# Optimization experiments

Measured on AMD Instinct MI355X. Metric: run time of the kernel, lower is better.

Reference implementation:

```python
import jax, jax.numpy as jnp
import numpy as np

P = 512       # protein_dim
D = 512       # drug_dim
N = 2000      # neighbors per layer
E = 300000    # binding edges per layer
ND = 100000   # total drugs
BASELINE = 6.0
LN_EPS = 1e-5


def setup_inputs() -> dict:
    key = jax.random.key(0)
    ks = jax.random.split(key, 24)
    inp = {
        "target_features": jax.random.normal(ks[0], (P,), jnp.float32),
        "form_features": jax.random.normal(ks[1], (N, P), jnp.float32),
        "role_features": jax.random.normal(ks[2], (N, P), jnp.float32),
        "form_neighbors": jnp.arange(N, dtype=jnp.int64) if jax.config.jax_enable_x64 else jnp.arange(N, dtype=jnp.int32),
        "role_neighbors": jnp.arange(N, dtype=jnp.int32),
        "form_binds_ei": jax.random.randint(ks[3], (2, E), 0, N, jnp.int32),
        "form_binds_y": jax.random.uniform(ks[4], (E,), jnp.float32) * 8.0 + 2.0,
        "role_binds_ei": jax.random.randint(ks[5], (2, E), 0, N, jnp.int32),
        "role_binds_y": jax.random.uniform(ks[6], (E,), jnp.float32) * 8.0 + 2.0,
        "drug_features": jax.random.normal(ks[7], (ND, D), jnp.float32),
    }
    inp["form_neighbors"] = jnp.arange(N, dtype=jnp.int32)
    attn_in = P * 2 + 16
    s1 = 1.0 / np.sqrt(attn_in)
    s2 = 1.0 / np.sqrt(64)
    sd = 1.0 / np.sqrt(D)
    sp = 1.0 / np.sqrt(P)
    inp["layer_emb"] = jax.random.normal(ks[8], (2, 16), jnp.float32)
    inp["W1"] = jax.random.uniform(ks[9], (attn_in, 64), jnp.float32, -s1, s1)
    inp["b1"] = jax.random.uniform(ks[10], (64,), jnp.float32, -s1, s1)
    inp["W2"] = jax.random.uniform(ks[11], (64, 1), jnp.float32, -s2, s2)
    inp["b2"] = jax.random.uniform(ks[12], (1,), jnp.float32, -s2, s2)
    inp["Wi1"] = jax.random.uniform(ks[13], (D, P), jnp.float32, -sd, sd)
    inp["bi1"] = jax.random.uniform(ks[14], (P,), jnp.float32, -sd, sd)
    inp["prelu_alpha"] = jnp.array(0.25, jnp.float32)
    inp["Wi2"] = jax.random.uniform(ks[15], (P, P), jnp.float32, -sp, sp)
    inp["bi2"] = jax.random.uniform(ks[16], (P,), jnp.float32, -sp, sp)
    inp["ln_gamma"] = jnp.ones((P,), jnp.float32)
    inp["ln_beta"] = jnp.zeros((P,), jnp.float32)
    return inp


def _pref_vectors(neighbor_ids, ei, y, drug_features):
    # Vectorized form of the per-neighbor masked gather-sum:
    # for each edge, find its neighbor slot (neighbor_ids is sorted);
    # edges whose src id is not a neighbor get zero weight.
    n = neighbor_ids.shape[0]
    pos = jnp.clip(jnp.searchsorted(neighbor_ids, ei[0]), 0, n - 1)
    valid = neighbor_ids[pos] == ei[0]
    w = jnp.where(valid, y - BASELINE, 0.0)              # [E]
    contrib = drug_features[ei[1]] * w[:, None]          # [E, D] gather (memory-bound)
    return jax.ops.segment_sum(contrib, pos, num_segments=n)  # [N, D]


def _attention(z_target, z_neighbors, l_vec, W1, b1, W2, b2):
    n = z_neighbors.shape[0]
    inp = jnp.concatenate(
        [jnp.broadcast_to(z_target, (n, z_target.shape[0])),
         z_neighbors,
         jnp.broadcast_to(l_vec, (n, l_vec.shape[0]))], axis=-1)  # [N, 2P+16]
    h = inp @ W1 + b1
    h = jnp.where(h > 0, h, 0.2 * h)  # LeakyReLU(0.2)
    return h @ W2 + b2                # [N, 1]


def reference(target_features, form_features, role_features, form_neighbors,
              role_neighbors, form_binds_ei, form_binds_y, role_binds_ei,
              role_binds_y, drug_features, layer_emb, W1, b1, W2, b2,
              Wi1, bi1, prelu_alpha, Wi2, bi2, ln_gamma, ln_beta):
    form_msgs = _pref_vectors(form_neighbors, form_binds_ei, form_binds_y, drug_features)
    role_msgs = _pref_vectors(role_neighbors, role_binds_ei, role_binds_y, drug_features)

    form_attn = _attention(target_features, form_features, layer_emb[0], W1, b1, W2, b2)
    role_attn = _attention(target_features, role_features, layer_emb[1], W1, b1, W2, b2)

    all_msgs = jnp.concatenate([form_msgs, role_msgs], axis=0)   # [2N, D]
    all_attn = jnp.concatenate([form_attn, role_attn], axis=0)   # [2N, 1]
    attn_weights = jax.nn.softmax(all_attn, axis=0)
    v_prior = jnp.sum(attn_weights * all_msgs, axis=0)           # [D]

    h = v_prior @ Wi1 + bi1
    h = jnp.where(h > 0, h, prelu_alpha * h)  # PReLU
    v = h @ Wi2 + bi2                          # [P]

    x = target_features + v
    mu = jnp.mean(x)
    var = jnp.mean(jnp.square(x - mu))
    z_refined = (x - mu) / jnp.sqrt(var + LN_EPS) * ln_gamma + ln_beta
    return (z_refined, form_msgs, role_msgs)
```

## Files before the change

### kernel.cpp

```cpp
#include <hip/hip_runtime.h>
#include <math.h>

static constexpr int PD = 512;
static constexpr float BASEV = 6.0f;
static constexpr int CAP = 320;

__global__ __launch_bounds__(256) void front_kernel(
    const int* __restrict__ ei_f, const float* __restrict__ y_f,
    const int* __restrict__ ei_r, const float* __restrict__ y_r,
    const int* __restrict__ nb_f, const int* __restrict__ nb_r,
    const float* __restrict__ target, const float* __restrict__ formF,
    const float* __restrict__ roleF, const float* __restrict__ lemb,
    const float* __restrict__ W1, const float* __restrict__ b1,
    const float* __restrict__ W2, const float* __restrict__ b2,
    int N, int E, int eb,
    int* __restrict__ cnt, int2* __restrict__ bins,
    float* __restrict__ logits) {
    int b = blockIdx.x;
    if (b < eb) {
        int i = b * 256 + threadIdx.x;
        if (i >= 2 * E) return;
        bool role = i >= E;
        int e = role ? i - E : i;
        const int* ei0 = role ? ei_r : ei_f;
        const int* ei1 = (role ? ei_r : ei_f) + E;
        int v = ei0[e];
        const int* nb = role ? nb_r : nb_f;
        int lo = 0, hi = N;
        while (lo < hi) { int mid = (lo + hi) >> 1; if (nb[mid] < v) lo = mid + 1; else hi = mid; }
        int pos = lo < N ? lo : N - 1;
        if (nb[pos] != v) return;
        int s = role ? N + pos : pos;
        float w = (role ? y_r[e] : y_f[e]) - BASEV;
        int slot = atomicAdd(&cnt[s], 1);
        if (slot < CAP) bins[(size_t)s * CAP + slot] = make_int2(ei1[e], __float_as_int(w));
    } else {
        int wave = threadIdx.x >> 6, lane = threadIdx.x & 63;
        int r0 = ((b - eb) * 4 + wave) * 8;
        int nseg = 2 * N;
        if (r0 >= nseg) return;
        const float* W1t = W1 + lane;
        float c = b1[lane];
        const float4* t4 = (const float4*)target;
        for (int p = 0; p < PD; p += 4) {
            float4 tv = t4[p >> 2];
            c += tv.x * W1t[(size_t)(p + 0) * 64] + tv.y * W1t[(size_t)(p + 1) * 64]
               + tv.z * W1t[(size_t)(p + 2) * 64] + tv.w * W1t[(size_t)(p + 3) * 64];
        }
        float c0 = c, c1 = c;
        for (int q = 0; q < 16; q++) {
            float wq = W1t[(size_t)(2 * PD + q) * 64];
            c0 += lemb[q] * wq;
            c1 += lemb[16 + q] * wq;
        }
        int nrows = nseg - r0; if (nrows > 8) nrows = 8;
        const float* z[8];
        float h[8];
#pragma unroll
        for (int r = 0; r < 8; r++) {
            int rr = r0 + (r < nrows ? r : 0);
            bool rl = rr >= N;
            z[r] = rl ? roleF + (size_t)(rr - N) * PD : formF + (size_t)rr * PD;
            h[r] = rl ? c1 : c0;
        }
        const float* W1z = W1 + (size_t)PD * 64 + lane;
        for (int p = 0; p < PD; p += 4) {
            float w0 = W1z[(size_t)(p + 0) * 64], w1 = W1z[(size_t)(p + 1) * 64];
            float w2 = W1z[(size_t)(p + 2) * 64], w3 = W1z[(size_t)(p + 3) * 64];
#pragma unroll
            for (int r = 0; r < 8; r++) {
                float4 zv = *(const float4*)(z[r] + p);
                h[r] += zv.x * w0 + zv.y * w1 + zv.z * w2 + zv.w * w3;
            }
        }
        float w2l = W2[lane];
#pragma unroll
        for (int r = 0; r < 8; r++) {
            float hh = h[r];
            hh = hh > 0.f ? hh : 0.2f * hh;
            float vv = hh * w2l;
#pragma unroll
            for (int off = 32; off > 0; off >>= 1) vv += __shfl_down(vv, off, 64);
            if (lane == 0 && r < nrows) logits[r0 + r] = vv + b2[0];
        }
    }
}

__global__ __launch_bounds__(128) void accum_kernel(const int* __restrict__ cnt,
                                                    const int2* __restrict__ bins,
                                                    const float* __restrict__ drug,
                                                    float* __restrict__ msgs) {
    int b = blockIdx.x;
    int t = threadIdx.x;
    int n = cnt[b]; n = n < CAP ? n : CAP;
    const int2* bb = bins + (size_t)b * CAP;
    float4 acc = make_float4(0.f, 0.f, 0.f, 0.f);
    int k = 0;
    for (; k + 7 < n; k += 8) {
        int2 e0 = bb[k + 0], e1 = bb[k + 1], e2 = bb[k + 2], e3 = bb[k + 3];
        int2 e4 = bb[k + 4], e5 = bb[k + 5], e6 = bb[k + 6], e7 = bb[k + 7];
        float4 d0 = ((const float4*)(drug + (size_t)e0.x * PD))[t];
        float4 d1 = ((const float4*)(drug + (size_t)e1.x * PD))[t];
        float4 d2 = ((const float4*)(drug + (size_t)e2.x * PD))[t];
        float4 d3 = ((const float4*)(drug + (size_t)e3.x * PD))[t];
        float4 d4 = ((const float4*)(drug + (size_t)e4.x * PD))[t];
        float4 d5 = ((const float4*)(drug + (size_t)e5.x * PD))[t];
        float4 d6 = ((const float4*)(drug + (size_t)e6.x * PD))[t];
        float4 d7 = ((const float4*)(drug + (size_t)e7.x * PD))[t];
        float w0 = __int_as_float(e0.y), w1 = __int_as_float(e1.y);
        float w2 = __int_as_float(e2.y), w3 = __int_as_float(e3.y);
        float w4 = __int_as_float(e4.y), w5 = __int_as_float(e5.y);
        float w6 = __int_as_float(e6.y), w7 = __int_as_float(e7.y);
        acc.x += w0 * d0.x; acc.y += w0 * d0.y; acc.z += w0 * d0.z; acc.w += w0 * d0.w;
        acc.x += w1 * d1.x; acc.y += w1 * d1.y; acc.z += w1 * d1.z; acc.w += w1 * d1.w;
        acc.x += w2 * d2.x; acc.y += w2 * d2.y; acc.z += w2 * d2.z; acc.w += w2 * d2.w;
        acc.x += w3 * d3.x; acc.y += w3 * d3.y; acc.z += w3 * d3.z; acc.w += w3 * d3.w;
        acc.x += w4 * d4.x; acc.y += w4 * d4.y; acc.z += w4 * d4.z; acc.w += w4 * d4.w;
        acc.x += w5 * d5.x; acc.y += w5 * d5.y; acc.z += w5 * d5.z; acc.w += w5 * d5.w;
        acc.x += w6 * d6.x; acc.y += w6 * d6.y; acc.z += w6 * d6.z; acc.w += w6 * d6.w;
        acc.x += w7 * d7.x; acc.y += w7 * d7.y; acc.z += w7 * d7.z; acc.w += w7 * d7.w;
    }
    for (; k < n; k++) {
        int2 e0 = bb[k];
        float w0 = __int_as_float(e0.y);
        float4 d0 = ((const float4*)(drug + (size_t)e0.x * PD))[t];
        acc.x += w0 * d0.x; acc.y += w0 * d0.y; acc.z += w0 * d0.z; acc.w += w0 * d0.w;
    }
    ((float4*)(msgs + (size_t)b * PD))[t] = acc;
}

__global__ __launch_bounds__(128) void vprior_kernel(const float* __restrict__ logits,
                                                     const float* __restrict__ msgs,
                                                     int nseg, float* __restrict__ v_prior) {
    __shared__ float red[128];
    int t = threadIdx.x;
    float m = -1e30f;
    for (int s = t; s < nseg; s += 128) m = fmaxf(m, logits[s]);
    red[t] = m; __syncthreads();
    for (int o = 64; o > 0; o >>= 1) { if (t < o) red[t] = fmaxf(red[t], red[t + o]); __syncthreads(); }
    m = red[0]; __syncthreads();
    float sum = 0.f;
    for (int s = t; s < nseg; s += 128) sum += expf(logits[s] - m);
    red[t] = sum; __syncthreads();
    for (int o = 64; o > 0; o >>= 1) { if (t < o) red[t] += red[t + o]; __syncthreads(); }
    float inv = 1.f / red[0];

    float4 acc = make_float4(0.f, 0.f, 0.f, 0.f);
    for (int s = blockIdx.x; s < nseg; s += gridDim.x) {
        float w = expf(logits[s] - m) * inv;
        float4 d = ((const float4*)(msgs + (size_t)s * PD))[t];
        acc.x += w * d.x; acc.y += w * d.y; acc.z += w * d.z; acc.w += w * d.w;
    }
    atomicAdd(&v_prior[4 * t + 0], acc.x);
    atomicAdd(&v_prior[4 * t + 1], acc.y);
    atomicAdd(&v_prior[4 * t + 2], acc.z);
    atomicAdd(&v_prior[4 * t + 3], acc.w);
}

__global__ __launch_bounds__(256) void mv1_kernel(const float* __restrict__ v_prior,
                                                  const float* __restrict__ Wi1,
                                                  float* __restrict__ h) {
    int b = blockIdx.x;
    int t = threadIdx.x;
    float2 acc = make_float2(0.f, 0.f);
    int d0 = b * 16;
    for (int d = d0; d < d0 + 16; d++) {
        float vd = v_prior[d];
        float2 w = ((const float2*)(Wi1 + (size_t)d * PD))[t];
        acc.x += vd * w.x; acc.y += vd * w.y;
    }
    atomicAdd(&h[2 * t + 0], acc.x);
    atomicAdd(&h[2 * t + 1], acc.y);
}

__global__ __launch_bounds__(256) void mv2_kernel(const float* __restrict__ h,
                                                  const float* __restrict__ bi1,
                                                  const float* __restrict__ alpha_p,
                                                  const float* __restrict__ Wi2,
                                                  float* __restrict__ v) {
    int b = blockIdx.x;
    int t = threadIdx.x;
    float alpha = alpha_p[0];
    float2 acc = make_float2(0.f, 0.f);
    int q0 = b * 16;
    for (int q = q0; q < q0 + 16; q++) {
        float hq = h[q] + bi1[q];
        hq = hq > 0.f ? hq : alpha * hq;
        float2 w = ((const float2*)(Wi2 + (size_t)q * PD))[t];
        acc.x += hq * w.x; acc.y += hq * w.y;
    }
    atomicAdd(&v[2 * t + 0], acc.x);
    atomicAdd(&v[2 * t + 1], acc.y);
}

__global__ __launch_bounds__(512) void final_kernel(const float* __restrict__ target,
                                                    const float* __restrict__ v,
                                                    const float* __restrict__ bi2,
                                                    const float* __restrict__ gamma,
                                                    const float* __restrict__ beta,
                                                    float* __restrict__ out) {
    __shared__ float red[512];
    int t = threadIdx.x;
    float x = target[t] + v[t] + bi2[t];
    red[t] = x; __syncthreads();
    for (int o = 256; o > 0; o >>= 1) { if (t < o) red[t] += red[t + o]; __syncthreads(); }
    float mu = red[0] * (1.f / 512.f);
    __syncthreads();
    float dx = x - mu;
    red[t] = dx * dx; __syncthreads();
    for (int o = 256; o > 0; o >>= 1) { if (t < o) red[t] += red[t + o]; __syncthreads(); }
    float var = red[0] * (1.f / 512.f);
    out[t] = dx * (1.f / sqrtf(var + 1e-5f)) * gamma[t] + beta[t];
}

extern "C" void kernel_launch(void* const* d_in, const int* in_sizes, int n_in,
                              void* d_out, int out_size, void* d_ws, size_t ws_size,
                              hipStream_t stream) {
    const float* target = (const float*)d_in[0];
    const float* formF  = (const float*)d_in[1];
    const float* roleF  = (const float*)d_in[2];
    const int*   nb_f   = (const int*)d_in[3];
    const int*   nb_r   = (const int*)d_in[4];
    const int*   ei_f   = (const int*)d_in[5];
    const float* y_f    = (const float*)d_in[6];
    const int*   ei_r   = (const int*)d_in[7];
    const float* y_r    = (const float*)d_in[8];
    const float* drug   = (const float*)d_in[9];
    const float* lemb   = (const float*)d_in[10];
    const float* W1     = (const float*)d_in[11];
    const float* b1     = (const float*)d_in[12];
    const float* W2     = (const float*)d_in[13];
    const float* b2     = (const float*)d_in[14];
    const float* Wi1    = (const float*)d_in[15];
    const float* bi1    = (const float*)d_in[16];
    const float* alpha  = (const float*)d_in[17];
    const float* Wi2    = (const float*)d_in[18];
    const float* bi2    = (const float*)d_in[19];
    const float* gamma  = (const float*)d_in[20];
    const float* beta   = (const float*)d_in[21];

    int N = in_sizes[3];
    int E = in_sizes[5] / 2;
    int nseg = 2 * N;

    int* ws = (int*)d_ws;
    int*   cnt     = ws + 0;
    float* v_prior = (float*)(ws + 4096);
    float* hbuf    = (float*)(ws + 4608);
    float* vbuf    = (float*)(ws + 5120);
    float* logits  = (float*)(ws + 5632);
    int2*  bins    = (int2*)(ws + 9728);

    float* out  = (float*)d_out;
    float* msgs = out + PD;

    hipMemsetAsync(ws, 0, 5632 * sizeof(int), stream);

    int EB = (2 * E + 255) / 256;
    int AB = (nseg + 31) / 32;
    front_kernel<<<EB + AB, 256, 0, stream>>>(ei_f, y_f, ei_r, y_r, nb_f, nb_r,
                                              target, formF, roleF, lemb,
                                              W1, b1, W2, b2, N, E, EB,
                                              cnt, bins, logits);
    accum_kernel<<<nseg, 128, 0, stream>>>(cnt, bins, drug, msgs);
    vprior_kernel<<<64, 128, 0, stream>>>(logits, msgs, nseg, v_prior);
    mv1_kernel<<<32, 256, 0, stream>>>(v_prior, Wi1, hbuf);
    mv2_kernel<<<32, 256, 0, stream>>>(hbuf, bi1, alpha, Wi2, vbuf);
    final_kernel<<<1, 512, 0, stream>>>(target, vbuf, bi2, gamma, beta, out);
}
```

Measured before the change: 523.5 us.

## Stage neighbor ids in LDS, batch binary searches, reorder blocks, halve attention rows

```diff
diff --git a/kernel.cpp b/kernel.cpp
--- a/kernel.cpp
+++ b/kernel.cpp
@@ -13,30 +13,67 @@
     const float* __restrict__ roleF, const float* __restrict__ lemb,
     const float* __restrict__ W1, const float* __restrict__ b1,
     const float* __restrict__ W2, const float* __restrict__ b2,
-    int N, int E, int eb,
+    int N, int E, int AB, int EBf,
     int* __restrict__ cnt, int2* __restrict__ bins,
     float* __restrict__ logits) {
+    __shared__ int snb[2048];
     int b = blockIdx.x;
-    if (b < eb) {
-        int i = b * 256 + threadIdx.x;
-        if (i >= 2 * E) return;
-        bool role = i >= E;
-        int e = role ? i - E : i;
-        const int* ei0 = role ? ei_r : ei_f;
-        const int* ei1 = (role ? ei_r : ei_f) + E;
-        int v = ei0[e];
+    if (b >= AB) {
+        int b2 = b - AB;
+        bool role = b2 >= EBf;
         const int* nb = role ? nb_r : nb_f;
-        int lo = 0, hi = N;
-        while (lo < hi) { int mid = (lo + hi) >> 1; if (nb[mid] < v) lo = mid + 1; else hi = mid; }
-        int pos = lo < N ? lo : N - 1;
-        if (nb[pos] != v) return;
-        int s = role ? N + pos : pos;
-        float w = (role ? y_r[e] : y_f[e]) - BASEV;
-        int slot = atomicAdd(&cnt[s], 1);
-        if (slot < CAP) bins[(size_t)s * CAP + slot] = make_int2(ei1[e], __float_as_int(w));
+        const int* ei = role ? ei_r : ei_f;
+        const float* yy = role ? y_r : y_f;
+        bool lds_ok = (N <= 2048);
+        if (lds_ok) {
+            for (int i = threadIdx.x; i < N; i += 256) snb[i] = nb[i];
+            __syncthreads();
+        }
+        int base = (role ? b2 - EBf : b2) * 1024;
+        int K = 32 - __clz(N);
+        int v[4], lo[4], hi[4], e[4];
+#pragma unroll
+        for (int r = 0; r < 4; r++) {
+            e[r] = base + threadIdx.x + r * 256;
+            bool a = e[r] < E;
+            v[r] = a ? ei[e[r]] : 0;
+            lo[r] = 0; hi[r] = a ? N : 0;
+        }
+        if (lds_ok) {
+            for (int it = 0; it < K; it++) {
+#pragma unroll
+                for (int r = 0; r < 4; r++) {
+                    if (lo[r] < hi[r]) {
+                        int mid = (lo[r] + hi[r]) >> 1;
+                        if (snb[mid] < v[r]) lo[r] = mid + 1; else hi[r] = mid;
+                    }
+                }
+            }
+        } else {
+            for (int it = 0; it < K; it++) {
+#pragma unroll
+                for (int r = 0; r < 4; r++) {
+                    if (lo[r] < hi[r]) {
+                        int mid = (lo[r] + hi[r]) >> 1;
+                        if (nb[mid] < v[r]) lo[r] = mid + 1; else hi[r] = mid;
+                    }
+                }
+            }
+        }
+#pragma unroll
+        for (int r = 0; r < 4; r++) {
+            if (e[r] >= E) continue;
+            int pos = lo[r] < N ? lo[r] : N - 1;
+            int nbp = lds_ok ? snb[pos] : nb[pos];
+            if (nbp != v[r]) continue;
+            int s = role ? N + pos : pos;
+            float w = yy[e[r]] - BASEV;
+            int slot = atomicAdd(&cnt[s], 1);
+            if (slot < CAP) bins[(size_t)s * CAP + slot] = make_int2(ei[E + e[r]], __float_as_int(w));
+        }
     } else {
         int wave = threadIdx.x >> 6, lane = threadIdx.x & 63;
-        int r0 = ((b - eb) * 4 + wave) * 8;
+        int r0 = (b * 4 + wave) * 4;
         int nseg = 2 * N;
         if (r0 >= nseg) return;
         const float* W1t = W1 + lane;
@@ -53,30 +90,32 @@
             c0 += lemb[q] * wq;
             c1 += lemb[16 + q] * wq;
         }
-        int nrows = nseg - r0; if (nrows > 8) nrows = 8;
-        const float* z[8];
-        float h[8];
-#pragma unroll
-        for (int r = 0; r < 8; r++) {
+        int nrows = nseg - r0; if (nrows > 4) nrows = 4;
+        const float* z[4];
+        float hA[4], hB[4];
+#pragma unroll
+        for (int r = 0; r < 4; r++) {
             int rr = r0 + (r < nrows ? r : 0);
             bool rl = rr >= N;
             z[r] = rl ? roleF + (size_t)(rr - N) * PD : formF + (size_t)rr * PD;
-            h[r] = rl ? c1 : c0;
+            hA[r] = rl ? c1 : c0;
+            hB[r] = 0.f;
         }
         const float* W1z = W1 + (size_t)PD * 64 + lane;
         for (int p = 0; p < PD; p += 4) {
             float w0 = W1z[(size_t)(p + 0) * 64], w1 = W1z[(size_t)(p + 1) * 64];
             float w2 = W1z[(size_t)(p + 2) * 64], w3 = W1z[(size_t)(p + 3) * 64];
 #pragma unroll
-            for (int r = 0; r < 8; r++) {
+            for (int r = 0; r < 4; r++) {
                 float4 zv = *(const float4*)(z[r] + p);
-                h[r] += zv.x * w0 + zv.y * w1 + zv.z * w2 + zv.w * w3;
+                hA[r] += zv.x * w0 + zv.y * w1;
+                hB[r] += zv.z * w2 + zv.w * w3;
             }
         }
         float w2l = W2[lane];
 #pragma unroll
-        for (int r = 0; r < 8; r++) {
-            float hh = h[r];
+        for (int r = 0; r < 4; r++) {
+            float hh = hA[r] + hB[r];
             hh = hh > 0.f ? hh : 0.2f * hh;
             float vv = hh * w2l;
 #pragma unroll
@@ -256,12 +295,12 @@
 
     hipMemsetAsync(ws, 0, 5632 * sizeof(int), stream);
 
-    int EB = (2 * E + 255) / 256;
-    int AB = (nseg + 31) / 32;
-    front_kernel<<<EB + AB, 256, 0, stream>>>(ei_f, y_f, ei_r, y_r, nb_f, nb_r,
-                                              target, formF, roleF, lemb,
-                                              W1, b1, W2, b2, N, E, EB,
-                                              cnt, bins, logits);
+    int AB  = (nseg + 15) / 16;
+    int EBf = (E + 1023) / 1024;
+    front_kernel<<<AB + 2 * EBf, 256, 0, stream>>>(ei_f, y_f, ei_r, y_r, nb_f, nb_r,
+                                                   target, formF, roleF, lemb,
+                                                   W1, b1, W2, b2, N, E, AB, EBf,
+                                                   cnt, bins, logits);
     accum_kernel<<<nseg, 128, 0, stream>>>(cnt, bins, drug, msgs);
     vprior_kernel<<<64, 128, 0, stream>>>(logits, msgs, nseg, v_prior);
     mv1_kernel<<<32, 256, 0, stream>>>(v_prior, Wi1, hbuf);
```

New measurement: 456.1 us. 1.15x faster.
